# Kernel optimization log

Hardware: AMD Instinct MI355X
Metric: run time of the kernel (lower is better)

Reference implementation:

```python
import jax, jax.numpy as jnp
import numpy as np


def _linear(x, W, b):
    # torch nn.Linear: y = x @ W.T + b, W is [out, in]
    return x @ W.T + b


def _sage_layer(x, edge_index, Ws, bs, Wn, bn):
    # GraphSAGE: mean-aggregate neighbor features via scatter-add, then two linears.
    src, tgt = edge_index[0], edge_index[1]
    N = x.shape[0]
    agg = jax.ops.segment_sum(x[src], tgt, num_segments=N)            # [N, D]
    deg = jax.ops.segment_sum(jnp.ones(src.shape, x.dtype), tgt, num_segments=N)  # [N]
    neighbor_mean = agg / jnp.maximum(deg, 1.0)[:, None]
    return _linear(x, Ws, bs) + _linear(neighbor_mean, Wn, bn)


def setup_inputs() -> dict:
    key = jax.random.key(0)
    ks = jax.random.split(key, 16)
    N, ATTR, H, OUT, E = 50000, 125, 128, 128, 800000
    IN = ATTR + 3
    s = 0.05
    inp = {
        "attr_features": jax.random.normal(ks[0], (N, ATTR), jnp.float32),
        "clustering_coefficient": jax.random.uniform(ks[1], (N, 1), jnp.float32),
        "bidirectional_links_ratio": jax.random.uniform(ks[2], (N, 1), jnp.float32),
        "exist_nodes": jnp.ones((N,), jnp.float32),
        "W_in": s * jax.random.normal(ks[3], (H, IN), jnp.float32),
        "b_in": s * jax.random.normal(ks[4], (H,), jnp.float32),
        "W1_self": s * jax.random.normal(ks[5], (H, H), jnp.float32),
        "b1_self": s * jax.random.normal(ks[6], (H,), jnp.float32),
        "W1_neigh": s * jax.random.normal(ks[7], (H, H), jnp.float32),
        "b1_neigh": s * jax.random.normal(ks[8], (H,), jnp.float32),
        "W2_self": s * jax.random.normal(ks[9], (OUT, H), jnp.float32),
        "b2_self": s * jax.random.normal(ks[10], (OUT,), jnp.float32),
        "W2_neigh": s * jax.random.normal(ks[11], (OUT, H), jnp.float32),
        "b2_neigh": s * jax.random.normal(ks[12], (OUT,), jnp.float32),
        "edge_index": jax.random.randint(ks[13], (2, E), 0, N, jnp.int64),
    }
    return inp


def reference(attr_features, clustering_coefficient, bidirectional_links_ratio,
              exist_nodes, W_in, b_in, W1_self, b1_self, W1_neigh, b1_neigh,
              W2_self, b2_self, W2_neigh, b2_neigh, edge_index):
    exist_col = exist_nodes[:, None]                                   # [N, 1]
    x = jnp.concatenate(
        [attr_features, clustering_coefficient, bidirectional_links_ratio, exist_col],
        axis=1)                                                        # [N, attr_dim+3]
    x = jax.nn.relu(_linear(x, W_in, b_in))                            # dropout=0 -> identity
    x = _sage_layer(x, edge_index, W1_self, b1_self, W1_neigh, b1_neigh)
    x = jax.nn.relu(x)
    x = x * exist_col
    x = _sage_layer(x, edge_index, W2_self, b2_self, W2_neigh, b2_neigh)
    return x * exist_col
```

## Files before the change

kernel.cpp:

```cpp
#include <hip/hip_runtime.h>

typedef __attribute__((ext_vector_type(8))) short short8;
typedef __attribute__((ext_vector_type(4))) float floatx4;

__device__ inline unsigned short f2bf(float f) {
    unsigned u = __float_as_uint(f);
    u += 0x7fffu + ((u >> 16) & 1u);
    return (unsigned short)(u >> 16);
}

#define CHUNK_CAP 12288
#define BTILE 2048
#define NPREP 256


__global__ __launch_bounds__(256, 4) void gemm0_bin(
    const float* __restrict__ attr, const float* __restrict__ cc,
    const float* __restrict__ bl, const float* __restrict__ ex,
    const float* __restrict__ Wf, const float* __restrict__ bias0,
    unsigned short* __restrict__ x1,
    const int* __restrict__ e, int* __restrict__ cursor,
    unsigned* __restrict__ packed_out,
    const float* __restrict__ w1s, const float* __restrict__ w1n,
    const float* __restrict__ w2s, const float* __restrict__ w2n,
    const float* __restrict__ b1s, const float* __restrict__ b1n,
    const float* __restrict__ b2s, const float* __restrict__ b2n,
    unsigned short* __restrict__ wb, float* __restrict__ biasf,
    int N, int ATTR, int E, int ntilesE, int gblk) {
    __shared__ __align__(16) char smem[18432];
    int t = threadIdx.x;
    int bid = blockIdx.x;

    if (bid >= gblk && bid < gblk + ntilesE) {
        unsigned* buf  = (unsigned*)smem;
        unsigned* sbuf = buf + BTILE;
        int* hist  = (int*)(sbuf + BTILE);
        int* offs  = hist + 128;
        int* gbase = offs + 128;
        int* lcur  = gbase + 128;
        int e0 = (bid - gblk) * BTILE;
        int cnt = min(BTILE, E - e0);
        if (t < 128) hist[t] = 0;
        __syncthreads();
        for (int j = t; j < cnt; j += 256) {
            unsigned src = (unsigned)e[e0 + j];
            unsigned tgt = (unsigned)e[E + e0 + j];
            unsigned c = tgt >> 9;
            buf[j] = (c << 25) | (src << 9) | (tgt & 511u);
            atomicAdd(&hist[c], 1);
        }
        __syncthreads();
        if (t < 128) offs[t] = hist[t];
        __syncthreads();
        for (int o = 1; o < 128; o <<= 1) {
            int v = (t < 128 && t >= o) ? offs[t - o] : 0;
            __syncthreads();
            if (t < 128) offs[t] += v;
            __syncthreads();
        }
        if (t < 128) {
            int excl = offs[t] - hist[t];
            offs[t] = excl;
            lcur[t] = excl;
            gbase[t] = (hist[t] > 0) ? t * CHUNK_CAP + atomicAdd(&cursor[t], hist[t]) : 0;
        }
        __syncthreads();
        for (int j = t; j < cnt; j += 256) {
            unsigned v = buf[j];
            int c = v >> 25;
            int p = atomicAdd(&lcur[c], 1);
            sbuf[p] = v;
        }
        __syncthreads();
        for (int j = t; j < cnt; j += 256) {
            unsigned v = sbuf[j];
            int c = v >> 25;
            packed_out[gbase[c] + (j - offs[c])] = v;
        }
        return;
    }

    if (bid >= gblk + ntilesE) {
        int pb = bid - gblk - ntilesE;
        int idx = pb * 256 + t;
        int m = idx >> 14, j = idx & 16383;
        const float* src = (m == 0) ? w1s : (m == 1) ? w1n : (m == 2) ? w2s : w2n;
        wb[idx] = f2bf(src[j]);
        if (pb == 0 && t < 128) {
            biasf[t]       = b1s[t] + b1n[t];
            biasf[128 + t] = b2s[t] + b2n[t];
        }
        return;
    }

    unsigned short* lx = (unsigned short*)smem;
    int lane = t & 63;
    int w = t >> 6;
    int node0 = bid * 64;
    int n_off = w * 32;
    int q = lane >> 4;
    int m16 = lane & 15;

    short8 bf[2][4];
    #pragma unroll
    for (int nt = 0; nt < 2; ++nt)
        #pragma unroll
        for (int kk = 0; kk < 4; ++kk) {
            const float* p = Wf + (n_off + nt * 16 + m16) * 128 + kk * 32 + q * 8;
            float4 aa = *(const float4*)p, bb = *(const float4*)(p + 4);
            short8 r;
            r[0] = (short)f2bf(aa.x); r[1] = (short)f2bf(aa.y);
            r[2] = (short)f2bf(aa.z); r[3] = (short)f2bf(aa.w);
            r[4] = (short)f2bf(bb.x); r[5] = (short)f2bf(bb.y);
            r[6] = (short)f2bf(bb.z); r[7] = (short)f2bf(bb.w);
            bf[nt][kk] = r;
        }

    floatx4 acc[4][2];
    #pragma unroll
    for (int nt = 0; nt < 2; ++nt) {
        float bv = bias0[n_off + nt * 16 + m16];
        floatx4 b4 = {bv, bv, bv, bv};
        #pragma unroll
        for (int mt = 0; mt < 4; ++mt) acc[mt][nt] = b4;
    }

    if (node0 + 64 > N) {
        for (int i = t; i < 64 * 136; i += 256) lx[i] = 0;
        __syncthreads();
    }

    #pragma unroll
    for (int i = 0; i < 8; ++i) {
        int idx = t + 256 * i;
        int nd = idx >> 5, g = idx & 31;
        int row = node0 + nd;
        int c0 = g * 4;
        if (row < N && c0 < ATTR) {
            if (c0 + 3 < ATTR) {
                float4 f = *(const float4*)(attr + (size_t)row * ATTR + c0);
                unsigned lo = (unsigned)f2bf(f.x) | ((unsigned)f2bf(f.y) << 16);
                unsigned hi = (unsigned)f2bf(f.z) | ((unsigned)f2bf(f.w) << 16);
                uint2 pk; pk.x = lo; pk.y = hi;
                *(uint2*)(lx + nd * 136 + c0) = pk;
            } else {
                for (int k = 0; k < 4; ++k) {
                    int cidx = c0 + k;
                    if (cidx < ATTR) lx[nd * 136 + cidx] = f2bf(attr[(size_t)row * ATTR + cidx]);
                }
            }
        }
    }
    {
        int nd = t >> 2, ci = t & 3;
        int row = node0 + nd;
        if (ci < 3 && row < N) {
            float v = (ci == 0) ? cc[row] : (ci == 1) ? bl[row] : ex[row];
            lx[nd * 136 + ATTR + ci] = f2bf(v);
        }
    }
    __syncthreads();

    #pragma unroll
    for (int kk = 0; kk < 4; ++kk) {
        short8 a[4];
        #pragma unroll
        for (int mt = 0; mt < 4; ++mt)
            a[mt] = *(const short8*)(lx + (mt * 16 + m16) * 136 + kk * 32 + q * 8);
        #pragma unroll
        for (int mt = 0; mt < 4; ++mt) {
            acc[mt][0] = __builtin_amdgcn_mfma_f32_16x16x32_bf16(a[mt], bf[0][kk], acc[mt][0], 0, 0, 0);
            acc[mt][1] = __builtin_amdgcn_mfma_f32_16x16x32_bf16(a[mt], bf[1][kk], acc[mt][1], 0, 0, 0);
        }
    }

    __syncthreads();
    #pragma unroll
    for (int mt = 0; mt < 4; ++mt)
        #pragma unroll
        for (int r = 0; r < 4; ++r) {
            int rl = mt * 16 + q * 4 + r;
            #pragma unroll
            for (int nt = 0; nt < 2; ++nt)
                lx[rl * 136 + n_off + nt * 16 + m16] = f2bf(fmaxf(acc[mt][nt][r], 0.0f));
        }
    __syncthreads();
    #pragma unroll
    for (int i = 0; i < 4; ++i) {
        int cidx = t + 256 * i;
        int nd = cidx >> 4, k = cidx & 15;
        int rr = node0 + nd;
        if (rr < N)
            *(uint4*)(x1 + (size_t)rr * 128 + k * 8) = *(const uint4*)(lx + nd * 136 + k * 8);
    }
}


__global__ __launch_bounds__(256) void chunk_csr(const unsigned* __restrict__ packed,
                                                 const int* __restrict__ cursor,
                                                 uint2* __restrict__ rows2,
                                                 int* __restrict__ colv, int N) {
    __shared__ int hist[512], offs[512], lcnt[512], pp[256];
    __shared__ int sbuf[CHUNK_CAP];
    int c = blockIdx.x;
    int base = c * CHUNK_CAP;
    int cnt = cursor[c];
    int t = threadIdx.x;
    hist[t] = 0;
    hist[t + 256] = 0;
    __syncthreads();
    for (int j = t; j < cnt; j += 256)
        atomicAdd(&hist[packed[base + j] & 511u], 1);
    __syncthreads();
    int a0 = hist[2 * t], a1 = hist[2 * t + 1];
    pp[t] = a0 + a1;
    __syncthreads();
    for (int o = 1; o < 256; o <<= 1) {
        int v = (t >= o) ? pp[t - o] : 0;
        __syncthreads();
        pp[t] += v;
        __syncthreads();
    }
    int excl = pp[t] - (a0 + a1);
    offs[2 * t] = excl;
    offs[2 * t + 1] = excl + a0;
    lcnt[2 * t] = 0;
    lcnt[2 * t + 1] = 0;
    __syncthreads();
    for (int j = t; j < 512; j += 256) {
        int node = c * 512 + j;
        if (node < N) {
            uint2 r;
            r.x = base + offs[j];
            r.y = base + offs[j] + hist[j];
            rows2[node] = r;
        }
    }
    for (int j = t; j < cnt; j += 256) {
        unsigned v = packed[base + j];
        int node = v & 511u;
        int p = offs[node] + atomicAdd(&lcnt[node], 1);
        sbuf[p] = (v >> 9) & 0xFFFFu;
    }
    __syncthreads();
    for (int j = t; j < cnt; j += 256) colv[base + j] = sbuf[j];
}


__global__ __launch_bounds__(256) void agg_mean(const unsigned short* __restrict__ x,
                                                const uint2* __restrict__ rows2,
                                                const int* __restrict__ colv,
                                                unsigned short* __restrict__ nm, int N) {
    int wid = (blockIdx.x * 256 + threadIdx.x) >> 6;
    int lane = threadIdx.x & 63;
    if (wid >= N) return;
    uint2 r = rows2[wid];
    int s0 = r.x, s1 = r.y;
    int deg = s1 - s0;
    int mn = deg < 64 ? deg : 64;
    int cvec = (lane < mn) ? colv[s0 + lane] : 0;
    int quarter = lane >> 4;
    int cl = (lane & 15) * 8;
    float a0 = 0.f, a1 = 0.f, a2 = 0.f, a3 = 0.f;
    float a4 = 0.f, a5 = 0.f, a6 = 0.f, a7 = 0.f;
    int lim = mn - 1;
    for (int j = 0; j < mn; j += 32) {
        uint4 v[8];
        #pragma unroll
        for (int u = 0; u < 8; ++u) {
            int ei = j + 4 * u + quarter;
            int idx = (ei <= lim) ? ei : lim;
            int s = __shfl(cvec, idx, 64);
            v[u] = *(const uint4*)(x + (size_t)s * 128 + cl);
        }
        #pragma unroll
        for (int u = 0; u < 8; ++u) {
            int ei = j + 4 * u + quarter;
            if (ei <= lim) {
                a0 += __uint_as_float(v[u].x << 16);
                a1 += __uint_as_float(v[u].x & 0xffff0000u);
                a2 += __uint_as_float(v[u].y << 16);
                a3 += __uint_as_float(v[u].y & 0xffff0000u);
                a4 += __uint_as_float(v[u].z << 16);
                a5 += __uint_as_float(v[u].z & 0xffff0000u);
                a6 += __uint_as_float(v[u].w << 16);
                a7 += __uint_as_float(v[u].w & 0xffff0000u);
            }
        }
    }
    for (int e = s0 + 64; e < s1; e += 4) {
        int ei = e + quarter;
        int idx = (ei < s1) ? ei : s1 - 1;
        int s = colv[idx];
        uint4 v = *(const uint4*)(x + (size_t)s * 128 + cl);
        if (ei < s1) {
            a0 += __uint_as_float(v.x << 16);
            a1 += __uint_as_float(v.x & 0xffff0000u);
            a2 += __uint_as_float(v.y << 16);
            a3 += __uint_as_float(v.y & 0xffff0000u);
            a4 += __uint_as_float(v.z << 16);
            a5 += __uint_as_float(v.z & 0xffff0000u);
            a6 += __uint_as_float(v.w << 16);
            a7 += __uint_as_float(v.w & 0xffff0000u);
        }
    }
    a0 += __shfl_xor(a0, 16, 64); a0 += __shfl_xor(a0, 32, 64);
    a1 += __shfl_xor(a1, 16, 64); a1 += __shfl_xor(a1, 32, 64);
    a2 += __shfl_xor(a2, 16, 64); a2 += __shfl_xor(a2, 32, 64);
    a3 += __shfl_xor(a3, 16, 64); a3 += __shfl_xor(a3, 32, 64);
    a4 += __shfl_xor(a4, 16, 64); a4 += __shfl_xor(a4, 32, 64);
    a5 += __shfl_xor(a5, 16, 64); a5 += __shfl_xor(a5, 32, 64);
    a6 += __shfl_xor(a6, 16, 64); a6 += __shfl_xor(a6, 32, 64);
    a7 += __shfl_xor(a7, 16, 64); a7 += __shfl_xor(a7, 32, 64);
    if (quarter == 0) {
        float inv = 1.0f / (float)(deg > 1 ? deg : 1);
        a0 *= inv; a1 *= inv; a2 *= inv; a3 *= inv;
        a4 *= inv; a5 *= inv; a6 *= inv; a7 *= inv;
        uint4 o;
        o.x = ((unsigned)f2bf(a1) << 16) | (unsigned)f2bf(a0);
        o.y = ((unsigned)f2bf(a3) << 16) | (unsigned)f2bf(a2);
        o.z = ((unsigned)f2bf(a5) << 16) | (unsigned)f2bf(a4);
        o.w = ((unsigned)f2bf(a7) << 16) | (unsigned)f2bf(a6);
        *(uint4*)(nm + (size_t)wid * 128 + cl) = o;
    }
}


__global__ __launch_bounds__(256, 3) void gemm_fused(
    const unsigned short* __restrict__ X0, const unsigned short* __restrict__ X1,
    const unsigned short* __restrict__ W0, const unsigned short* __restrict__ W1,
    const float* __restrict__ bias, const float* __restrict__ ex,
    unsigned short* __restrict__ obf, float* __restrict__ of32,
    int N, int relu) {
    __shared__ __align__(16) unsigned short lx[64 * 136];
    int tid = threadIdx.x;
    int lane = tid & 63;
    int w = tid >> 6;
    int node0 = blockIdx.x * 64;
    int n_off = w * 32;
    int q = lane >> 4;
    int m16 = lane & 15;

    short8 bf0[2][4], bf1[2][4];
    #pragma unroll
    for (int nt = 0; nt < 2; ++nt)
        #pragma unroll
        for (int kk = 0; kk < 4; ++kk) {
            bf0[nt][kk] = *(const short8*)(W0 + (n_off + nt * 16 + m16) * 128 + kk * 32 + q * 8);
            bf1[nt][kk] = *(const short8*)(W1 + (n_off + nt * 16 + m16) * 128 + kk * 32 + q * 8);
        }

    floatx4 acc[4][2];
    #pragma unroll
    for (int nt = 0; nt < 2; ++nt) {
        float bv = bias[n_off + nt * 16 + m16];
        floatx4 b4 = {bv, bv, bv, bv};
        #pragma unroll
        for (int mt = 0; mt < 4; ++mt) acc[mt][nt] = b4;
    }

    for (int ph = 0; ph < 2; ++ph) {
        const unsigned short* X = ph ? X1 : X0;
        for (int i = 0; i < 4; ++i) {
            int c = tid + 256 * i;
            int nd = c >> 4, ck = c & 15;
            short8 v = {0, 0, 0, 0, 0, 0, 0, 0};
            if (node0 + nd < N) v = *(const short8*)(X + (size_t)(node0 + nd) * 128 + ck * 8);
            *(short8*)(lx + nd * 136 + ck * 8) = v;
        }
        __syncthreads();
        #pragma unroll
        for (int kk = 0; kk < 4; ++kk) {
            short8 a[4];
            #pragma unroll
            for (int mt = 0; mt < 4; ++mt)
                a[mt] = *(const short8*)(lx + (mt * 16 + m16) * 136 + kk * 32 + q * 8);
            #pragma unroll
            for (int mt = 0; mt < 4; ++mt) {
                const short8* p0 = ph ? &bf1[0][kk] : &bf0[0][kk];
                const short8* p1 = ph ? &bf1[1][kk] : &bf0[1][kk];
                acc[mt][0] = __builtin_amdgcn_mfma_f32_16x16x32_bf16(a[mt], *p0, acc[mt][0], 0, 0, 0);
                acc[mt][1] = __builtin_amdgcn_mfma_f32_16x16x32_bf16(a[mt], *p1, acc[mt][1], 0, 0, 0);
            }
        }
        __syncthreads();
    }

    if (obf) {
        #pragma unroll
        for (int mt = 0; mt < 4; ++mt)
            #pragma unroll
            for (int r = 0; r < 4; ++r) {
                int rl = mt * 16 + q * 4 + r;
                int rr = node0 + rl;
                float e = (rr < N) ? ex[rr] : 0.0f;
                #pragma unroll
                for (int nt = 0; nt < 2; ++nt) {
                    float v = acc[mt][nt][r];
                    if (relu) v = fmaxf(v, 0.0f);
                    lx[rl * 136 + n_off + nt * 16 + m16] = f2bf(v * e);
                }
            }
        __syncthreads();
        #pragma unroll
        for (int i = 0; i < 4; ++i) {
            int cidx = tid + 256 * i;
            int nd = cidx >> 4, k = cidx & 15;
            int rr = node0 + nd;
            if (rr < N)
                *(uint4*)(obf + (size_t)rr * 128 + k * 8) = *(const uint4*)(lx + nd * 136 + k * 8);
        }
    } else {
        float* C = (float*)lx;
        #pragma unroll
        for (int pass = 0; pass < 2; ++pass) {
            if ((w >> 1) == pass) {
                #pragma unroll
                for (int mt = 0; mt < 4; ++mt)
                    #pragma unroll
                    for (int r = 0; r < 4; ++r) {
                        int rl = mt * 16 + q * 4 + r;
                        int rr = node0 + rl;
                        float e = (rr < N) ? ex[rr] : 0.0f;
                        #pragma unroll
                        for (int nt = 0; nt < 2; ++nt) {
                            float v = acc[mt][nt][r];
                            if (relu) v = fmaxf(v, 0.0f);
                            int colL = (w & 1) * 32 + nt * 16 + m16;
                            C[rl * 66 + colL] = v * e;
                        }
                    }
            }
            __syncthreads();
            #pragma unroll
            for (int i = 0; i < 4; ++i) {
                int g = tid + 256 * i;
                int nd = g >> 4, k = g & 15;
                int rr = node0 + nd;
                if (rr < N)
                    *(float4*)(of32 + (size_t)rr * 128 + pass * 64 + k * 4) =
                        *(const float4*)(C + nd * 66 + k * 4);
            }
            __syncthreads();
        }
    }
}


extern "C" void kernel_launch(void* const* d_in, const int* in_sizes, int n_in,
                              void* d_out, int out_size, void* d_ws, size_t ws_size,
                              hipStream_t stream) {
    const float* attr = (const float*)d_in[0];
    const float* cc   = (const float*)d_in[1];
    const float* bl   = (const float*)d_in[2];
    const float* ex   = (const float*)d_in[3];
    const float* w_in = (const float*)d_in[4];
    const float* b_in = (const float*)d_in[5];
    const float* w1s  = (const float*)d_in[6];
    const float* b1s  = (const float*)d_in[7];
    const float* w1n  = (const float*)d_in[8];
    const float* b1n  = (const float*)d_in[9];
    const float* w2s  = (const float*)d_in[10];
    const float* b2s  = (const float*)d_in[11];
    const float* w2n  = (const float*)d_in[12];
    const float* b2n  = (const float*)d_in[13];
    const int*   eidx = (const int*)d_in[14];

    int N = in_sizes[3];
    int ATTR = in_sizes[0] / N;
    int E = in_sizes[14] / 2;
    int Npad = ((N + 63) / 64) * 64;
    int nchunk = (N + 511) / 512;
    int ntilesE = (E + BTILE - 1) / BTILE;
    int gblk = Npad / 64;

    char* ws = (char*)d_ws;
    size_t off = 0;
    auto alloc = [&](size_t bytes) -> char* {
        off = (off + 255) & ~(size_t)255;
        char* p = ws + off;
        off += bytes;
        return p;
    };
    unsigned short* x1 = (unsigned short*)alloc((size_t)Npad * 128 * 2);
    unsigned short* x2 = (unsigned short*)alloc((size_t)Npad * 128 * 2);
    unsigned short* nm = (unsigned short*)alloc((size_t)Npad * 128 * 2);
    int* colv        = (int*)alloc((size_t)nchunk * CHUNK_CAP * 4);
    unsigned* packed = (unsigned*)alloc((size_t)nchunk * CHUNK_CAP * 4);
    uint2* rows2     = (uint2*)alloc((size_t)N * 8);
    int* cursor      = (int*)alloc(128 * 4);
    unsigned short* wb = (unsigned short*)alloc((size_t)4 * 16384 * 2);
    float* biasf     = (float*)alloc(256 * 4);

    hipMemsetAsync(cursor, 0, 128 * sizeof(int), stream);

    gemm0_bin<<<gblk + ntilesE + NPREP, 256, 0, stream>>>(
        attr, cc, bl, ex, w_in, b_in, x1,
        eidx, cursor, packed,
        w1s, w1n, w2s, w2n, b1s, b1n, b2s, b2n, wb, biasf,
        N, ATTR, E, ntilesE, gblk);
    chunk_csr<<<nchunk, 256, 0, stream>>>(packed, cursor, rows2, colv, N);
    agg_mean<<<(N + 3) / 4, 256, 0, stream>>>(x1, rows2, colv, nm, N);
    gemm_fused<<<gblk, 256, 0, stream>>>(x1, nm, wb, wb + 16384,
                                         biasf, ex, x2, (float*)nullptr, N, 1);
    agg_mean<<<(N + 3) / 4, 256, 0, stream>>>(x2, rows2, colv, nm, N);
    gemm_fused<<<gblk, 256, 0, stream>>>(x2, nm, wb + 2 * 16384, wb + 3 * 16384,
                                         biasf + 128, ex, (unsigned short*)nullptr,
                                         (float*)d_out, N, 0);
}
```

Before: 236.7 us.

## Widen CSR build block, predicate gathers, and stage both GEMM inputs at once

chunk_csr now runs 512 threads, one per node slot, which simplifies the prefix scan and the rows2 write. agg_mean skips the global load for out-of-range edge slots instead of loading a clamped duplicate. gemm_fused loads both input tiles into a doubled LDS buffer before any compute, which removes a barrier pair and lets the loads overlap the weight fetch. Its fp32 epilogue also writes the full 128-column tile in one pass. The larger LDS footprint may lower occupancy for gemm_fused.

```diff
diff --git a/kernel.cpp b/kernel.cpp
--- a/kernel.cpp
+++ b/kernel.cpp
@@ -196,54 +196,48 @@
 }
 
 
-__global__ __launch_bounds__(256) void chunk_csr(const unsigned* __restrict__ packed,
+__global__ __launch_bounds__(512) void chunk_csr(const unsigned* __restrict__ packed,
                                                  const int* __restrict__ cursor,
                                                  uint2* __restrict__ rows2,
                                                  int* __restrict__ colv, int N) {
-    __shared__ int hist[512], offs[512], lcnt[512], pp[256];
+    __shared__ int hist[512], offs[512], lcnt[512];
     __shared__ int sbuf[CHUNK_CAP];
     int c = blockIdx.x;
     int base = c * CHUNK_CAP;
     int cnt = cursor[c];
     int t = threadIdx.x;
     hist[t] = 0;
-    hist[t + 256] = 0;
-    __syncthreads();
-    for (int j = t; j < cnt; j += 256)
+    __syncthreads();
+    for (int j = t; j < cnt; j += 512)
         atomicAdd(&hist[packed[base + j] & 511u], 1);
     __syncthreads();
-    int a0 = hist[2 * t], a1 = hist[2 * t + 1];
-    pp[t] = a0 + a1;
-    __syncthreads();
-    for (int o = 1; o < 256; o <<= 1) {
-        int v = (t >= o) ? pp[t - o] : 0;
-        __syncthreads();
-        pp[t] += v;
-        __syncthreads();
-    }
-    int excl = pp[t] - (a0 + a1);
-    offs[2 * t] = excl;
-    offs[2 * t + 1] = excl + a0;
-    lcnt[2 * t] = 0;
-    lcnt[2 * t + 1] = 0;
-    __syncthreads();
-    for (int j = t; j < 512; j += 256) {
-        int node = c * 512 + j;
-        if (node < N) {
-            uint2 r;
-            r.x = base + offs[j];
-            r.y = base + offs[j] + hist[j];
-            rows2[node] = r;
-        }
-    }
-    for (int j = t; j < cnt; j += 256) {
+    offs[t] = hist[t];
+    __syncthreads();
+    for (int o = 1; o < 512; o <<= 1) {
+        int v = (t >= o) ? offs[t - o] : 0;
+        __syncthreads();
+        offs[t] += v;
+        __syncthreads();
+    }
+    int excl = offs[t] - hist[t];
+    int node = c * 512 + t;
+    if (node < N) {
+        uint2 r;
+        r.x = base + excl;
+        r.y = base + excl + hist[t];
+        rows2[node] = r;
+    }
+    offs[t] = excl;
+    lcnt[t] = 0;
+    __syncthreads();
+    for (int j = t; j < cnt; j += 512) {
         unsigned v = packed[base + j];
-        int node = v & 511u;
-        int p = offs[node] + atomicAdd(&lcnt[node], 1);
+        int nd = v & 511u;
+        int p = offs[nd] + atomicAdd(&lcnt[nd], 1);
         sbuf[p] = (v >> 9) & 0xFFFFu;
     }
     __syncthreads();
-    for (int j = t; j < cnt; j += 256) colv[base + j] = sbuf[j];
+    for (int j = t; j < cnt; j += 512) colv[base + j] = sbuf[j];
 }
 
 
@@ -269,9 +263,9 @@
         #pragma unroll
         for (int u = 0; u < 8; ++u) {
             int ei = j + 4 * u + quarter;
-            int idx = (ei <= lim) ? ei : lim;
-            int s = __shfl(cvec, idx, 64);
-            v[u] = *(const uint4*)(x + (size_t)s * 128 + cl);
+            int s = __shfl(cvec, (ei <= lim) ? ei : lim, 64);
+            if (ei <= lim)
+                v[u] = *(const uint4*)(x + (size_t)s * 128 + cl);
         }
         #pragma unroll
         for (int u = 0; u < 8; ++u) {
@@ -292,8 +286,8 @@
         int ei = e + quarter;
         int idx = (ei < s1) ? ei : s1 - 1;
         int s = colv[idx];
-        uint4 v = *(const uint4*)(x + (size_t)s * 128 + cl);
         if (ei < s1) {
+            uint4 v = *(const uint4*)(x + (size_t)s * 128 + cl);
             a0 += __uint_as_float(v.x << 16);
             a1 += __uint_as_float(v.x & 0xffff0000u);
             a2 += __uint_as_float(v.y << 16);
@@ -332,7 +326,7 @@
     const float* __restrict__ bias, const float* __restrict__ ex,
     unsigned short* __restrict__ obf, float* __restrict__ of32,
     int N, int relu) {
-    __shared__ __align__(16) unsigned short lx[64 * 136];
+    __shared__ __align__(16) unsigned short lx[2 * 64 * 136];
     int tid = threadIdx.x;
     int lane = tid & 63;
     int w = tid >> 6;
@@ -341,40 +335,48 @@
     int q = lane >> 4;
     int m16 = lane & 15;
 
-    short8 bf0[2][4], bf1[2][4];
-    #pragma unroll
-    for (int nt = 0; nt < 2; ++nt)
-        #pragma unroll
-        for (int kk = 0; kk < 4; ++kk) {
-            bf0[nt][kk] = *(const short8*)(W0 + (n_off + nt * 16 + m16) * 128 + kk * 32 + q * 8);
-            bf1[nt][kk] = *(const short8*)(W1 + (n_off + nt * 16 + m16) * 128 + kk * 32 + q * 8);
-        }
-
-    floatx4 acc[4][2];
-    #pragma unroll
-    for (int nt = 0; nt < 2; ++nt) {
-        float bv = bias[n_off + nt * 16 + m16];
-        floatx4 b4 = {bv, bv, bv, bv};
-        #pragma unroll
-        for (int mt = 0; mt < 4; ++mt) acc[mt][nt] = b4;
-    }
-
+    #pragma unroll
     for (int ph = 0; ph < 2; ++ph) {
         const unsigned short* X = ph ? X1 : X0;
+        unsigned short* L = lx + ph * 64 * 136;
+        #pragma unroll
         for (int i = 0; i < 4; ++i) {
             int c = tid + 256 * i;
             int nd = c >> 4, ck = c & 15;
             short8 v = {0, 0, 0, 0, 0, 0, 0, 0};
             if (node0 + nd < N) v = *(const short8*)(X + (size_t)(node0 + nd) * 128 + ck * 8);
-            *(short8*)(lx + nd * 136 + ck * 8) = v;
-        }
-        __syncthreads();
+            *(short8*)(L + nd * 136 + ck * 8) = v;
+        }
+    }
+
+    short8 bf0[2][4], bf1[2][4];
+    #pragma unroll
+    for (int nt = 0; nt < 2; ++nt)
+        #pragma unroll
+        for (int kk = 0; kk < 4; ++kk) {
+            bf0[nt][kk] = *(const short8*)(W0 + (n_off + nt * 16 + m16) * 128 + kk * 32 + q * 8);
+            bf1[nt][kk] = *(const short8*)(W1 + (n_off + nt * 16 + m16) * 128 + kk * 32 + q * 8);
+        }
+
+    floatx4 acc[4][2];
+    #pragma unroll
+    for (int nt = 0; nt < 2; ++nt) {
+        float bv = bias[n_off + nt * 16 + m16];
+        floatx4 b4 = {bv, bv, bv, bv};
+        #pragma unroll
+        for (int mt = 0; mt < 4; ++mt) acc[mt][nt] = b4;
+    }
+    __syncthreads();
+
+    #pragma unroll
+    for (int ph = 0; ph < 2; ++ph) {
+        const unsigned short* L = lx + ph * 64 * 136;
         #pragma unroll
         for (int kk = 0; kk < 4; ++kk) {
             short8 a[4];
             #pragma unroll
             for (int mt = 0; mt < 4; ++mt)
-                a[mt] = *(const short8*)(lx + (mt * 16 + m16) * 136 + kk * 32 + q * 8);
+                a[mt] = *(const short8*)(L + (mt * 16 + m16) * 136 + kk * 32 + q * 8);
             #pragma unroll
             for (int mt = 0; mt < 4; ++mt) {
                 const short8* p0 = ph ? &bf1[0][kk] : &bf0[0][kk];
@@ -383,8 +385,8 @@
                 acc[mt][1] = __builtin_amdgcn_mfma_f32_16x16x32_bf16(a[mt], *p1, acc[mt][1], 0, 0, 0);
             }
         }
-        __syncthreads();
-    }
+    }
+    __syncthreads();
 
     if (obf) {
         #pragma unroll
@@ -413,35 +415,27 @@
     } else {
         float* C = (float*)lx;
         #pragma unroll
-        for (int pass = 0; pass < 2; ++pass) {
-            if ((w >> 1) == pass) {
+        for (int mt = 0; mt < 4; ++mt)
+            #pragma unroll
+            for (int r = 0; r < 4; ++r) {
+                int rl = mt * 16 + q * 4 + r;
+                int rr = node0 + rl;
+                float e = (rr < N) ? ex[rr] : 0.0f;
                 #pragma unroll
-                for (int mt = 0; mt < 4; ++mt)
-                    #pragma unroll
-                    for (int r = 0; r < 4; ++r) {
-                        int rl = mt * 16 + q * 4 + r;
-                        int rr = node0 + rl;
-                        float e = (rr < N) ? ex[rr] : 0.0f;
-                        #pragma unroll
-                        for (int nt = 0; nt < 2; ++nt) {
-                            float v = acc[mt][nt][r];
-                            if (relu) v = fmaxf(v, 0.0f);
-                            int colL = (w & 1) * 32 + nt * 16 + m16;
-                            C[rl * 66 + colL] = v * e;
-                        }
-                    }
+                for (int nt = 0; nt < 2; ++nt) {
+                    float v = acc[mt][nt][r];
+                    if (relu) v = fmaxf(v, 0.0f);
+                    C[rl * 132 + n_off + nt * 16 + m16] = v * e;
+                }
             }
-            __syncthreads();
-            #pragma unroll
-            for (int i = 0; i < 4; ++i) {
-                int g = tid + 256 * i;
-                int nd = g >> 4, k = g & 15;
-                int rr = node0 + nd;
-                if (rr < N)
-                    *(float4*)(of32 + (size_t)rr * 128 + pass * 64 + k * 4) =
-                        *(const float4*)(C + nd * 66 + k * 4);
-            }
-            __syncthreads();
+        __syncthreads();
+        #pragma unroll
+        for (int i = 0; i < 8; ++i) {
+            int g = tid + 256 * i;
+            int nd = g >> 5, k = g & 31;
+            int rr = node0 + nd;
+            if (rr < N)
+                *(float4*)(of32 + (size_t)rr * 128 + k * 4) = *(const float4*)(C + nd * 132 + k * 4);
         }
     }
 }
@@ -499,7 +493,7 @@
         eidx, cursor, packed,
         w1s, w1n, w2s, w2n, b1s, b1n, b2s, b2n, wb, biasf,
         N, ATTR, E, ntilesE, gblk);
-    chunk_csr<<<nchunk, 256, 0, stream>>>(packed, cursor, rows2, colv, N);
+    chunk_csr<<<nchunk, 512, 0, stream>>>(packed, cursor, rows2, colv, N);
     agg_mean<<<(N + 3) / 4, 256, 0, stream>>>(x1, rows2, colv, nm, N);
     gemm_fused<<<gblk, 256, 0, stream>>>(x1, nm, wb, wb + 16384,
                                          biasf, ex, x2, (float*)nullptr, N, 1);
```

Measured after the change: 219.3 us. 7.3% less time.
